# Optimization experiments

Hardware: AMD Instinct MI355X
Metric: run time of the kernel (lower is better)

## Reference

```python
import jax, jax.numpy as jnp
import numpy as np
from jax import lax

N, L, C_IN, NOISE_C, COMP, NC = 256, 512, 514, 112, 16, 2
MAIN_IN = NOISE_C + COMP  # 128
FEAT = NC * 4 * L         # 4096

def _conv1d(x, w, b, pad):
    # x [N,C,L], w [O,I,K]
    y = lax.conv_general_dilated(x, w, (1,), [(pad, pad)], dimension_numbers=('NCH', 'OIH', 'NCH'))
    return y + b[None, :, None]

def _bn(x, g, b):
    # BatchNorm1d, training mode: biased batch stats over (N, L)
    m = x.mean(axis=(0, 2), keepdims=True)
    v = x.var(axis=(0, 2), keepdims=True)
    return (x - m) * lax.rsqrt(v + 1e-5) * g[None, :, None] + b[None, :, None]

def _lrelu(x):
    return jnp.where(x >= 0, x, 0.2 * x)

def _pos_encode(length, dim):
    j = np.arange(dim)
    div = 1.0 / np.power(10000.0, 2 * (j[:, None] // 2) / dim)   # [dim,1]
    ang = np.arange(length)[None, :] * div                       # [dim,length]
    ang = np.where((j % 2 == 0)[:, None], np.sin(ang), np.cos(ang))
    return jnp.asarray(ang[None], jnp.float32)                   # [1,dim,length]

def _assemble(circle_prob, slider_prob):
    # Vectorized run-length label expansion equivalent to the per-sample python while-loop.
    # circle_prob [N, L/2, 2], slider_prob [N, L/4, 2] -> [N, L, 3]
    n, B = slider_prob.shape[0], slider_prob.shape[1]
    c = jnp.argmax(circle_prob, -1)
    s = jnp.argmax(slider_prob, -1)
    zc = jnp.zeros(circle_prob.shape[:-1] + (1,), circle_prob.dtype)
    zs = jnp.zeros(slider_prob.shape[:-1] + (1,), slider_prob.dtype)
    cp3 = jnp.concatenate([circle_prob, zc], -1)                                   # insert 0 at class 2
    sp3 = jnp.concatenate([slider_prob[..., :1], zs, slider_prob[..., 1:]], -1)    # insert 0 at class 1
    pad100 = jnp.array([1., 0., 0.], cp3.dtype)
    pad001 = jnp.array([0., 0., 1.], cp3.dtype)
    bidx = jnp.arange(B)[None, :]
    # slider-body blocks: slider run continues and not cut by sequence end
    body = (s == 1) & (bidx < B - 1)
    prev_body = jnp.concatenate([jnp.zeros((n, 1), bool), body[:, :-1]], 1)
    # tail block ends a slider run (either run stops, or boundary block)
    tail = ((s == 1) & (bidx == B - 1)) | ((s == 0) & prev_body)
    # circle emission for each half-step: prob row if predicted circle else pad
    cr0 = jnp.where((c == 1)[..., None], cp3, pad100).reshape(n, B, 2, 3)
    bodyE = body[..., None]
    row0 = jnp.where((body | tail)[..., None], sp3, cr0[:, :, 0, :])
    row1 = jnp.where(bodyE, pad001, pad100)
    row2 = jnp.where(bodyE, pad001, cr0[:, :, 1, :])
    row3 = jnp.where(bodyE, pad001, pad100)
    return jnp.stack([row0, row1, row2, row3], 2).reshape(n, 4 * B, 3)

def _forward(noise, cond_data, gumbel_u, ext_w1, ext_b1, ext_w2, ext_b2, ext_bn_g, ext_bn_b,
             m_w1, m_b1, m_w2, m_b2, m_bn_g, m_bn_b, lin_w, lin_b, circ_w, circ_b, slid_w, slid_b):
    # FeatureExtractor
    x = cond_data.transpose(0, 2, 1)                      # [N, 514, L]
    x = _lrelu(_conv1d(x, ext_w1, ext_b1, 0))             # [N, 32, L]
    cond = _bn(_conv1d(x, ext_w2, ext_b2, 1), ext_bn_g, ext_bn_b)  # [N, 16, L]
    gen_in = jnp.concatenate([cond, noise.transpose(0, 2, 1)], 1) + _pos_encode(L, MAIN_IN)  # [N,128,L]
    h = _lrelu(_conv1d(gen_in, m_w1, m_b1, 3))            # [N, 32, L]
    h = _lrelu(_bn(_conv1d(h, m_w2, m_b2, 1), m_bn_g, m_bn_b))     # [N, 8, L]
    flat = _lrelu(h.reshape(h.shape[0], -1) @ lin_w + lin_b)       # [N, 4096]
    circle_prob = (flat @ circ_w + circ_b).reshape(-1, L // 2, NC)
    slider_prob = (flat @ slid_w + slid_b).reshape(-1, L // 4, NC)
    out = _assemble(circle_prob, slider_prob)             # [N, L, 3]
    # gumbel_softmax(hard=True, tau=1)
    g = -jnp.log(-jnp.log(gumbel_u + 1e-10) + 1e-10)
    logits = out + g
    y_soft = jax.nn.softmax(logits, -1)
    y_hard = jax.nn.one_hot(jnp.argmax(logits, -1), 3, dtype=y_soft.dtype)
    gen_out = y_hard + y_soft - lax.stop_gradient(y_soft)
    return gen_out, cond

def setup_inputs() -> dict:
    key = jax.random.key(0)
    ks = jax.random.split(key, 12)
    def rn(k, shape, fan_in):
        return jax.random.normal(k, shape, jnp.float32) * (1.0 / fan_in) ** 0.5
    return {
        'noise': jax.random.normal(ks[0], (N, L, NOISE_C), jnp.float32),
        'cond_data': jax.random.normal(ks[1], (N, L, C_IN), jnp.float32),
        'gumbel_u': jax.random.uniform(ks[2], (N, L, 3), jnp.float32),
        'ext_w1': rn(ks[3], (C_IN // 16, C_IN, 1), C_IN), 'ext_b1': jnp.zeros(C_IN // 16),
        'ext_w2': rn(ks[4], (COMP, C_IN // 16, 3), 3 * (C_IN // 16)), 'ext_b2': jnp.zeros(COMP),
        'ext_bn_g': jnp.ones(COMP), 'ext_bn_b': jnp.zeros(COMP),
        'm_w1': rn(ks[5], (NC * 16, MAIN_IN, 7), 7 * MAIN_IN), 'm_b1': jnp.zeros(NC * 16),
        'm_w2': rn(ks[6], (NC * 4, NC * 16, 3), 3 * NC * 16), 'm_b2': jnp.zeros(NC * 4),
        'm_bn_g': jnp.ones(NC * 4), 'm_bn_b': jnp.zeros(NC * 4),
        'lin_w': rn(ks[7], (FEAT, FEAT), FEAT), 'lin_b': jnp.zeros(FEAT),
        'circ_w': rn(ks[8], (FEAT, NC * L // 2), FEAT), 'circ_b': jnp.zeros(NC * L // 2),
        'slid_w': rn(ks[9], (FEAT, NC * L // 4), FEAT), 'slid_b': jnp.zeros(NC * L // 4),
    }

def reference(noise, cond_data, gumbel_u, ext_w1, ext_b1, ext_w2, ext_b2, ext_bn_g, ext_bn_b,
              m_w1, m_b1, m_w2, m_b2, m_bn_g, m_bn_b, lin_w, lin_b, circ_w, circ_b, slid_w, slid_b):
    return _forward(noise, cond_data, gumbel_u, ext_w1, ext_b1, ext_w2, ext_b2, ext_bn_g, ext_bn_b,
                    m_w1, m_b1, m_w2, m_b2, m_bn_g, m_bn_b, lin_w, lin_b, circ_w, circ_b, slid_w, slid_b)
```

## Files before the change

kernel.cpp:

```cpp
#include <hip/hip_runtime.h>
#include <math.h>

#define NB 256
#define LL 512
#define CIN 514

__device__ __forceinline__ float lrelu(float x) { return x >= 0.f ? x : 0.2f * x; }

__global__ __launch_bounds__(256) void k_pos(float* __restrict__ pos) {
    int idx = blockIdx.x * 256 + threadIdx.x;
    int c = idx >> 9, l = idx & 511;
    double e = (double)(2 * (c >> 1)) / 128.0;
    double dv = 1.0 / pow(10000.0, e);
    double a = (double)l * dv;
    pos[idx] = (float)((c & 1) ? cos(a) : sin(a));
}

__global__ __launch_bounds__(256) void k_posconv(const float* __restrict__ POS, const float* __restrict__ W,
                                                 const float* __restrict__ bias, float* __restrict__ PC) {
    const int t = threadIdx.x;
    const int o = blockIdx.x >> 4, l0 = (blockIdx.x & 15) * 32;
    const int l = l0 + (t & 31), cs = t >> 5;
    float acc = 0.f;
    for (int ci = 0; ci < 16; ++ci) {
        int c = cs * 16 + ci;
        float wv[7];
#pragma unroll
        for (int k = 0; k < 7; ++k) wv[k] = W[o * 896 + c * 7 + k];
#pragma unroll
        for (int k = 0; k < 7; ++k) {
            int gl = l + k - 3;
            if (gl >= 0 && gl < LL) acc += wv[k] * POS[c * LL + gl];
        }
    }
    __shared__ float red[8][33];
    red[cs][t & 31] = acc;
    __syncthreads();
    if (cs == 0) {
        float s = bias[o];
#pragma unroll
        for (int j = 0; j < 8; ++j) s += red[j][t & 31];
        PC[o * LL + l0 + (t & 31)] = s;
    }
}

__global__ __launch_bounds__(256) void k_conv1(const float* __restrict__ X, const float* __restrict__ W,
                                               float* __restrict__ Pbase) {
    __shared__ __align__(16) float As[16][524];
    __shared__ __align__(16) float Bs[16][36];
    const int t = threadIdx.x;
    const int n = blockIdx.x >> 2, z = blockIdx.x & 3;
    const int kbase = z * 128;
    const int nch = (z == 3) ? 9 : 8;
    const int tl = t & 63, to = t >> 6;
    const size_t rowbase = (size_t)n * 512 * CIN;

    float acc[8][8];
#pragma unroll
    for (int oi = 0; oi < 8; ++oi)
#pragma unroll
        for (int p = 0; p < 8; ++p) acc[oi][p] = 0.f;

    float2 pf[16];
    float2 pfb;

    {
        const int kb = kbase;
#pragma unroll
        for (int ps = 0; ps < 16; ++ps) {
            int idx = ps * 256 + t;
            int pos = idx >> 3, kp = idx & 7;
            int gk = kb + kp * 2;
            float2 v = {0.f, 0.f};
            if (gk + 1 < CIN) v = *(const float2*)(X + rowbase + (size_t)pos * CIN + gk);
            else if (gk < CIN) v.x = X[rowbase + (size_t)pos * CIN + gk];
            pf[ps] = v;
        }
        {
            int o = t >> 3, kp = t & 7;
            int gk = kb + kp * 2;
            float2 v = {0.f, 0.f};
            if (gk + 1 < CIN) v = *(const float2*)(W + (size_t)o * CIN + gk);
            else if (gk < CIN) v.x = W[(size_t)o * CIN + gk];
            pfb = v;
        }
#pragma unroll
        for (int ps = 0; ps < 16; ++ps) {
            int idx = ps * 256 + t;
            int pos = idx >> 3, kp = idx & 7;
            As[kp * 2][pos] = pf[ps].x;
            As[kp * 2 + 1][pos] = pf[ps].y;
        }
        {
            int o = t >> 3, kp = t & 7;
            Bs[kp * 2][o] = pfb.x;
            Bs[kp * 2 + 1][o] = pfb.y;
        }
    }
    __syncthreads();

    for (int c = 0; c < nch; ++c) {
        if (c + 1 < nch) {
            const int kb = kbase + (c + 1) * 16;
#pragma unroll
            for (int ps = 0; ps < 16; ++ps) {
                int idx = ps * 256 + t;
                int pos = idx >> 3, kp = idx & 7;
                int gk = kb + kp * 2;
                float2 v = {0.f, 0.f};
                if (gk + 1 < CIN) v = *(const float2*)(X + rowbase + (size_t)pos * CIN + gk);
                else if (gk < CIN) v.x = X[rowbase + (size_t)pos * CIN + gk];
                pf[ps] = v;
            }
            int o = t >> 3, kp = t & 7;
            int gk = kb + kp * 2;
            float2 v = {0.f, 0.f};
            if (gk + 1 < CIN) v = *(const float2*)(W + (size_t)o * CIN + gk);
            else if (gk < CIN) v.x = W[(size_t)o * CIN + gk];
            pfb = v;
        }
#pragma unroll
        for (int kk = 0; kk < 16; ++kk) {
            float4 aL = *(const float4*)&As[kk][tl * 4];
            float4 aH = *(const float4*)&As[kk][256 + tl * 4];
            float4 b0 = *(const float4*)&Bs[kk][to * 8];
            float4 b1 = *(const float4*)&Bs[kk][to * 8 + 4];
            float av[8] = {aL.x, aL.y, aL.z, aL.w, aH.x, aH.y, aH.z, aH.w};
            float bv[8] = {b0.x, b0.y, b0.z, b0.w, b1.x, b1.y, b1.z, b1.w};
#pragma unroll
            for (int oi = 0; oi < 8; ++oi)
#pragma unroll
                for (int p = 0; p < 8; ++p) acc[oi][p] += av[p] * bv[oi];
        }
        __syncthreads();
        if (c + 1 < nch) {
#pragma unroll
            for (int ps = 0; ps < 16; ++ps) {
                int idx = ps * 256 + t;
                int pos = idx >> 3, kp = idx & 7;
                As[kp * 2][pos] = pf[ps].x;
                As[kp * 2 + 1][pos] = pf[ps].y;
            }
            int o = t >> 3, kp = t & 7;
            Bs[kp * 2][o] = pfb.x;
            Bs[kp * 2 + 1][o] = pfb.y;
        }
        __syncthreads();
    }

    float* P = Pbase + (size_t)z * 4194304;
#pragma unroll
    for (int oi = 0; oi < 8; ++oi) {
        int o = to * 8 + oi;
        float4 v0 = {acc[oi][0], acc[oi][1], acc[oi][2], acc[oi][3]};
        float4 v1 = {acc[oi][4], acc[oi][5], acc[oi][6], acc[oi][7]};
        *(float4*)(P + ((size_t)n * 32 + o) * LL + tl * 4) = v0;
        *(float4*)(P + ((size_t)n * 32 + o) * LL + 256 + tl * 4) = v1;
    }
}

__global__ __launch_bounds__(256) void k_conv2(const float* __restrict__ Pbase,
                                               const float* __restrict__ b1, const float* __restrict__ W,
                                               const float* __restrict__ bias, float* __restrict__ out) {
    __shared__ __align__(16) float Xs[32][264];
    __shared__ __align__(16) float Ws[16][32][4];
    const int t = threadIdx.x;
    const int n = blockIdx.x >> 1, l0 = (blockIdx.x & 1) * 256;
    for (int idx = t; idx < 32 * 258; idx += 256) {
        int i = idx / 258, j = idx % 258;
        int gl = l0 - 1 + j;
        float v = 0.f;
        if (gl >= 0 && gl < LL) {
            size_t off = ((size_t)n * 32 + i) * LL + gl;
            v = lrelu(Pbase[off] + Pbase[off + 4194304] + Pbase[off + 8388608] + Pbase[off + 12582912] + b1[i]);
        }
        Xs[i][j] = v;
    }
    for (int idx = t; idx < 1536; idx += 256) {
        int o = idx / 96, r = idx % 96;
        Ws[o][r / 3][r % 3] = W[idx];
    }
    __syncthreads();
    const int tx = t & 31, ty = t >> 5;
    float acc[2][8];
#pragma unroll
    for (int q = 0; q < 2; ++q)
#pragma unroll
        for (int p = 0; p < 8; ++p) acc[q][p] = 0.f;
    for (int i = 0; i < 32; ++i) {
        float4 a0 = *(const float4*)&Xs[i][tx*8];
        float4 a1 = *(const float4*)&Xs[i][tx*8+4];
        float4 a2 = *(const float4*)&Xs[i][tx*8+8];
        float a[12] = {a0.x,a0.y,a0.z,a0.w,a1.x,a1.y,a1.z,a1.w,a2.x,a2.y,a2.z,a2.w};
#pragma unroll
        for (int q = 0; q < 2; ++q) {
            float4 b = *(const float4*)&Ws[ty*2+q][i][0];
#pragma unroll
            for (int p = 0; p < 8; ++p)
                acc[q][p] += a[p]*b.x + a[p+1]*b.y + a[p+2]*b.z;
        }
    }
#pragma unroll
    for (int q = 0; q < 2; ++q) {
        int o = ty*2+q; float bb = bias[o];
#pragma unroll
        for (int h = 0; h < 2; ++h) {
            float4 v;
            v.x = acc[q][h*4+0] + bb; v.y = acc[q][h*4+1] + bb;
            v.z = acc[q][h*4+2] + bb; v.w = acc[q][h*4+3] + bb;
            *(float4*)(out + ((size_t)n*16 + o)*LL + l0 + tx*8 + h*4) = v;
        }
    }
}

__global__ __launch_bounds__(256) void k_redstats(const float* __restrict__ src, int C, float* __restrict__ part) {
    const int ch = blockIdx.x, sl = blockIdx.y, t = threadIdx.x;
    float s = 0.f, q = 0.f;
    for (int i = t; i < 4096; i += 256) {
        int n = sl*8 + (i >> 9), l = i & 511;
        float v = src[((size_t)n*C + ch)*LL + l];
        s += v; q += v*v;
    }
    __shared__ float rs[256], rq[256];
    rs[t] = s; rq[t] = q;
    __syncthreads();
    for (int off = 128; off > 0; off >>= 1) {
        if (t < off) { rs[t] += rs[t+off]; rq[t] += rq[t+off]; }
        __syncthreads();
    }
    if (t == 0) { part[(ch*32+sl)*2] = rs[0]; part[(ch*32+sl)*2+1] = rq[0]; }
}

__global__ void k_bnfinal(const float* __restrict__ part, const float* __restrict__ g,
                          const float* __restrict__ b, int C, float* __restrict__ ss) {
    int ch = threadIdx.x;
    if (ch >= C) return;
    float s = 0.f, q = 0.f;
    for (int j = 0; j < 32; ++j) { s += part[(ch*32 + j)*2]; q += part[(ch*32 + j)*2 + 1]; }
    float mean = s * (1.f/131072.f);
    float var = q * (1.f/131072.f) - mean*mean;
    float sc = g[ch] / sqrtf(var + 1e-5f);
    ss[ch] = sc;
    ss[C + ch] = b[ch] - mean * sc;
}

__global__ __launch_bounds__(256) void k_bnapply(const float* __restrict__ src, const float* __restrict__ ss,
        int C, float* __restrict__ dst, int act, int total4) {
    int i4 = blockIdx.x * 256 + threadIdx.x;
    if (i4 >= total4) return;
    int i = i4 << 2;
    int ch = (i >> 9) % C;
    float sc = ss[ch], sh = ss[C + ch];
    float4 v = reinterpret_cast<const float4*>(src)[i4];
    v.x = v.x*sc + sh; v.y = v.y*sc + sh; v.z = v.z*sc + sh; v.w = v.w*sc + sh;
    if (act) { v.x = lrelu(v.x); v.y = lrelu(v.y); v.z = lrelu(v.z); v.w = lrelu(v.w); }
    reinterpret_cast<float4*>(dst)[i4] = v;
}

__global__ __launch_bounds__(256) void k_mconv1(const float* __restrict__ C16, const float* __restrict__ NZ,
        const float* __restrict__ PC, const float* __restrict__ W,
        float* __restrict__ out0, float* __restrict__ out1) {
    __shared__ __align__(16) float Gs[16][268];
    __shared__ __align__(16) float Ws[32][16][8];
    const int t = threadIdx.x;
    const int n = blockIdx.x >> 2, l0 = ((blockIdx.x >> 1) & 1) * 256, z = blockIdx.x & 1;
    const int tx = t & 31, ty = t >> 5;
    float acc[4][8];
#pragma unroll
    for (int q = 0; q < 4; ++q)
#pragma unroll
        for (int p = 0; p < 8; ++p) acc[q][p] = 0.f;

    float gpf[17];
    float wpf[14];

    if (z == 0) {
        for (int idx = t; idx < 16*262; idx += 256) {
            int c = idx / 262, j = idx - c*262;
            int gl = l0 - 3 + j;
            float v = 0.f;
            if (gl >= 0 && gl < LL) v = C16[((size_t)n*16 + c)*LL + gl];
            Gs[c][j] = v;
        }
#pragma unroll
        for (int p = 0; p < 14; ++p) {
            int idx = p * 256 + t;
            int o = idx / 112, r = idx - o * 112;
            Ws[o][r / 7][r % 7] = W[(size_t)o*896 + r];
        }
    } else {
#pragma unroll
        for (int p = 0; p < 17; ++p) {
            int idx = p * 256 + t;
            float v = 0.f;
            if (idx < 4192) {
                int c = idx & 15, j = idx >> 4;
                int gl = l0 - 3 + j;
                if (gl >= 0 && gl < LL) v = NZ[((size_t)n*LL + gl)*112 + 48 + c];
            }
            gpf[p] = v;
        }
#pragma unroll
        for (int p = 0; p < 14; ++p) {
            int idx = p * 256 + t;
            int o = idx / 112, r = idx - o * 112;
            wpf[p] = W[(size_t)o*896 + 4*112 + r];
        }
#pragma unroll
        for (int p = 0; p < 17; ++p) {
            int idx = p * 256 + t;
            if (idx < 4192) Gs[idx & 15][idx >> 4] = gpf[p];
        }
#pragma unroll
        for (int p = 0; p < 14; ++p) {
            int idx = p * 256 + t;
            int o = idx / 112, r = idx - o * 112;
            Ws[o][r / 7][r % 7] = wpf[p];
        }
    }
    __syncthreads();

    for (int cc = 0; cc < 4; ++cc) {
        if (cc < 3) {
            const int nctg = z * 4 + cc + 1;
            const int nc0 = nctg * 16 - 16;
#pragma unroll
            for (int p = 0; p < 17; ++p) {
                int idx = p * 256 + t;
                float v = 0.f;
                if (idx < 4192) {
                    int c = idx & 15, j = idx >> 4;
                    int gl = l0 - 3 + j;
                    if (gl >= 0 && gl < LL) v = NZ[((size_t)n*LL + gl)*112 + nc0 + c];
                }
                gpf[p] = v;
            }
#pragma unroll
            for (int p = 0; p < 14; ++p) {
                int idx = p * 256 + t;
                int o = idx / 112, r = idx - o * 112;
                wpf[p] = W[(size_t)o*896 + nctg*112 + r];
            }
        }
        for (int ci = 0; ci < 16; ++ci) {
            float4 a0 = *(const float4*)&Gs[ci][tx*4];
            float4 a1 = *(const float4*)&Gs[ci][tx*4+4];
            float4 a2 = *(const float4*)&Gs[ci][tx*4+8];
            float4 a3 = *(const float4*)&Gs[ci][128+tx*4];
            float4 a4 = *(const float4*)&Gs[ci][128+tx*4+4];
            float4 a5 = *(const float4*)&Gs[ci][128+tx*4+8];
            float aA[12] = {a0.x,a0.y,a0.z,a0.w,a1.x,a1.y,a1.z,a1.w,a2.x,a2.y,a2.z,a2.w};
            float aB[12] = {a3.x,a3.y,a3.z,a3.w,a4.x,a4.y,a4.z,a4.w,a5.x,a5.y,a5.z,a5.w};
#pragma unroll
            for (int q = 0; q < 4; ++q) {
                float4 b0 = *(const float4*)&Ws[ty*4+q][ci][0];
                float4 b1 = *(const float4*)&Ws[ty*4+q][ci][4];
                float b[7] = {b0.x,b0.y,b0.z,b0.w,b1.x,b1.y,b1.z};
#pragma unroll
                for (int p = 0; p < 4; ++p) {
#pragma unroll
                    for (int k = 0; k < 7; ++k) {
                        acc[q][p]   += aA[p+k]*b[k];
                        acc[q][4+p] += aB[p+k]*b[k];
                    }
                }
            }
        }
        if (cc < 3) {
            __syncthreads();
#pragma unroll
            for (int p = 0; p < 17; ++p) {
                int idx = p * 256 + t;
                if (idx < 4192) Gs[idx & 15][idx >> 4] = gpf[p];
            }
#pragma unroll
            for (int p = 0; p < 14; ++p) {
                int idx = p * 256 + t;
                int o = idx / 112, r = idx - o * 112;
                Ws[o][r / 7][r % 7] = wpf[p];
            }
            __syncthreads();
        }
    }

    float* out = z ? out1 : out0;
#pragma unroll
    for (int q = 0; q < 4; ++q) {
        int o = ty*4 + q;
        float4 p0 = {0.f,0.f,0.f,0.f}, p1 = {0.f,0.f,0.f,0.f};
        if (z == 0) {
            p0 = *(const float4*)(PC + o*LL + l0 + tx*4);
            p1 = *(const float4*)(PC + o*LL + l0 + 128 + tx*4);
        }
        float4 v0 = {acc[q][0]+p0.x, acc[q][1]+p0.y, acc[q][2]+p0.z, acc[q][3]+p0.w};
        float4 v1 = {acc[q][4]+p1.x, acc[q][5]+p1.y, acc[q][6]+p1.z, acc[q][7]+p1.w};
        *(float4*)(out + ((size_t)n*32 + o)*LL + l0 + tx*4) = v0;
        *(float4*)(out + ((size_t)n*32 + o)*LL + l0 + 128 + tx*4) = v1;
    }
}

__global__ __launch_bounds__(256) void k_mconv2(const float* __restrict__ P0, const float* __restrict__ P1,
        const float* __restrict__ W, const float* __restrict__ bias, float* __restrict__ out) {
    __shared__ __align__(16) float Xs[32][264];
    __shared__ __align__(16) float Ws[8][32][4];
    const int t = threadIdx.x;
    const int n = blockIdx.x >> 1, l0 = (blockIdx.x & 1) * 256;
    for (int idx = t; idx < 32 * 258; idx += 256) {
        int i = idx / 258, j = idx % 258;
        int gl = l0 - 1 + j;
        float v = 0.f;
        if (gl >= 0 && gl < LL) {
            size_t off = ((size_t)n * 32 + i) * LL + gl;
            v = lrelu(P0[off] + P1[off]);
        }
        Xs[i][j] = v;
    }
    for (int idx = t; idx < 768; idx += 256) {
        int o = idx / 96, r = idx % 96;
        Ws[o][r / 3][r % 3] = W[idx];
    }
    __syncthreads();
    const int tx = t & 31, ty = t >> 5;
    float acc[8];
#pragma unroll
    for (int p = 0; p < 8; ++p) acc[p] = 0.f;
    for (int i = 0; i < 32; ++i) {
        float4 a0 = *(const float4*)&Xs[i][tx*8];
        float4 a1 = *(const float4*)&Xs[i][tx*8+4];
        float4 a2 = *(const float4*)&Xs[i][tx*8+8];
        float a[12] = {a0.x,a0.y,a0.z,a0.w,a1.x,a1.y,a1.z,a1.w,a2.x,a2.y,a2.z,a2.w};
        float4 b = *(const float4*)&Ws[ty][i][0];
#pragma unroll
        for (int p = 0; p < 8; ++p)
            acc[p] += a[p]*b.x + a[p+1]*b.y + a[p+2]*b.z;
    }
    float bb = bias[ty];
#pragma unroll
    for (int h = 0; h < 2; ++h) {
        float4 v;
        v.x = acc[h*4+0] + bb; v.y = acc[h*4+1] + bb;
        v.z = acc[h*4+2] + bb; v.w = acc[h*4+3] + bb;
        *(float4*)(out + ((size_t)n*8 + ty)*LL + l0 + tx*8 + h*4) = v;
    }
}

__global__ __launch_bounds__(256) void k_lin(const float* __restrict__ A, const float* __restrict__ B,
                                             float* __restrict__ part) {
    __shared__ __align__(16) float As[16][132];
    __shared__ __align__(16) float Bs[16][132];
    const int t = threadIdx.x;
    const int bid = blockIdx.x;
    const int xcd = bid & 7, j = bid >> 3;
    const int z = j >> 3;
    const int m0 = ((j >> 2) & 1) * 128;
    const int f0 = (xcd * 4 + (j & 3)) * 128;
    const int k0base = z * 256;
    const int sar = t & 127, saq = t >> 7;
    const int sbr = t >> 4, sbq = t & 15;
    const int mq = (t & 15) * 4, fq = (t >> 4) * 4;

    float acc[8][8];
#pragma unroll
    for (int i = 0; i < 8; ++i)
#pragma unroll
        for (int q = 0; q < 8; ++q) acc[i][q] = 0.f;

    for (int it = 0; it < 16; ++it) {
        const int k0 = k0base + it * 16;
        {
            const float* pA = A + (size_t)(m0 + sar) * 4096 + k0 + saq * 8;
            float4 a0 = *(const float4*)(pA);
            float4 a1 = *(const float4*)(pA + 4);
            const float* pB = B + (size_t)(k0 + sbr) * 4096 + f0 + sbq * 8;
            float4 b0 = *(const float4*)(pB);
            float4 b1 = *(const float4*)(pB + 4);
            As[saq*8+0][sar] = a0.x; As[saq*8+1][sar] = a0.y; As[saq*8+2][sar] = a0.z; As[saq*8+3][sar] = a0.w;
            As[saq*8+4][sar] = a1.x; As[saq*8+5][sar] = a1.y; As[saq*8+6][sar] = a1.z; As[saq*8+7][sar] = a1.w;
            *(float4*)&Bs[sbr][sbq*8] = b0;
            *(float4*)&Bs[sbr][sbq*8+4] = b1;
        }
        __syncthreads();
#pragma unroll
        for (int kk = 0; kk < 16; ++kk) {
            float4 a0 = *(const float4*)&As[kk][mq];
            float4 a1 = *(const float4*)&As[kk][mq + 64];
            float4 b0 = *(const float4*)&Bs[kk][fq];
            float4 b1 = *(const float4*)&Bs[kk][fq + 64];
            float av[8] = {a0.x,a0.y,a0.z,a0.w,a1.x,a1.y,a1.z,a1.w};
            float bv[8] = {b0.x,b0.y,b0.z,b0.w,b1.x,b1.y,b1.z,b1.w};
#pragma unroll
            for (int i = 0; i < 8; ++i)
#pragma unroll
                for (int q = 0; q < 8; ++q) acc[i][q] += av[i] * bv[q];
        }
        __syncthreads();
    }

#pragma unroll
    for (int i = 0; i < 8; ++i) {
        int m = m0 + mq + (i & 3) + (i >> 2) * 64;
        float4 v0 = {acc[i][0], acc[i][1], acc[i][2], acc[i][3]};
        float4 v1 = {acc[i][4], acc[i][5], acc[i][6], acc[i][7]};
        *(float4*)(part + ((size_t)z * 256 + m) * 4096 + f0 + fq) = v0;
        *(float4*)(part + ((size_t)z * 256 + m) * 4096 + f0 + fq + 64) = v1;
    }
}

__global__ __launch_bounds__(256) void k_linred(const float* __restrict__ part, const float* __restrict__ bias,
        float* __restrict__ out) {
    int i4 = blockIdx.x*256 + threadIdx.x;
    int i = i4 << 2;
    int f = i & 4095;
    float4 s = *(const float4*)(bias + f);
#pragma unroll
    for (int zz = 0; zz < 16; ++zz) {
        float4 p = ((const float4*)(part + (size_t)zz * 1048576))[i4];
        s.x += p.x; s.y += p.y; s.z += p.z; s.w += p.w;
    }
    float4 r;
    r.x = lrelu(s.x); r.y = lrelu(s.y); r.z = lrelu(s.z); r.w = lrelu(s.w);
    ((float4*)out)[i4] = r;
}

__global__ __launch_bounds__(256) void k_heads(const float* __restrict__ A, const float* __restrict__ CW,
        const float* __restrict__ SW, float* __restrict__ part) {
    __shared__ __align__(16) float As[32][36];
    __shared__ __align__(16) float Bs[32][132];
    const int t = threadIdx.x;
    const int m0 = blockIdx.x * 32, f0 = blockIdx.y * 128, z = blockIdx.z;
    const float* B; int ldb, fb;
    if (f0 < 512) { B = CW; ldb = 512; fb = f0; } else { B = SW; ldb = 256; fb = f0 - 512; }
    const int tm = t & 7, tf = t >> 3;
    const int mi = t >> 3, kq = t & 7;
    float acc[4][4];
#pragma unroll
    for (int pm = 0; pm < 4; ++pm)
#pragma unroll
        for (int pf = 0; pf < 4; ++pf) acc[pm][pf] = 0.f;
    for (int k0 = z * 256; k0 < z * 256 + 256; k0 += 32) {
        float4 av = *(const float4*)(A + (size_t)(m0 + mi) * 4096 + k0 + kq * 4);
        As[kq*4+0][mi] = av.x; As[kq*4+1][mi] = av.y; As[kq*4+2][mi] = av.z; As[kq*4+3][mi] = av.w;
#pragma unroll
        for (int pass = 0; pass < 4; ++pass) {
            int fi = pass * 32 + kq * 4;
            *(float4*)&Bs[mi][fi] = *(const float4*)(B + (size_t)(k0 + mi) * ldb + fb + fi);
        }
        __syncthreads();
#pragma unroll 8
        for (int kk = 0; kk < 32; ++kk) {
            float4 a = *(const float4*)&As[kk][tm * 4];
            float4 b = *(const float4*)&Bs[kk][tf * 4];
            float avv[4] = {a.x,a.y,a.z,a.w};
            float bvv[4] = {b.x,b.y,b.z,b.w};
#pragma unroll
            for (int pm = 0; pm < 4; ++pm)
#pragma unroll
                for (int pf = 0; pf < 4; ++pf) acc[pm][pf] += avv[pm]*bvv[pf];
        }
        __syncthreads();
    }
#pragma unroll
    for (int pm = 0; pm < 4; ++pm) {
        float4 v = {acc[pm][0], acc[pm][1], acc[pm][2], acc[pm][3]};
        *(float4*)(part + ((size_t)z * 256 + m0 + tm * 4 + pm) * 768 + f0 + tf * 4) = v;
    }
}

__global__ __launch_bounds__(256) void k_headred(const float* __restrict__ part, const float* __restrict__ cb,
        const float* __restrict__ sb, float* __restrict__ circ, float* __restrict__ slid) {
    int i4 = blockIdx.x * 256 + threadIdx.x;
    int i = i4 << 2;
    int n = i / 768, f = i % 768;
    float4 s = {0.f,0.f,0.f,0.f};
#pragma unroll
    for (int ks = 0; ks < 16; ++ks) {
        float4 p = *(const float4*)(part + ((size_t)ks*256 + n)*768 + f);
        s.x += p.x; s.y += p.y; s.z += p.z; s.w += p.w;
    }
    if (f < 512) {
        float4 bb = *(const float4*)(cb + f);
        s.x += bb.x; s.y += bb.y; s.z += bb.z; s.w += bb.w;
        *(float4*)(circ + (size_t)n*512 + f) = s;
    } else {
        float4 bb = *(const float4*)(sb + f - 512);
        s.x += bb.x; s.y += bb.y; s.z += bb.z; s.w += bb.w;
        *(float4*)(slid + (size_t)n*256 + f - 512) = s;
    }
}

__global__ __launch_bounds__(128) void k_assemble(const float* __restrict__ circ, const float* __restrict__ slid,
        const float* __restrict__ gum, float* __restrict__ out) {
    const int n = blockIdx.x;
    const int b = threadIdx.x;
    const float* sp = slid + (size_t)n * 256;
    const float* cp = circ + (size_t)n * 512;
    float sl0 = sp[2*b], sl1 = sp[2*b+1];
    int s = sl1 > sl0 ? 1 : 0;
    int prevb = 0;
    if (b > 0) prevb = (sp[2*b-1] > sp[2*b-2]) ? 1 : 0;
    bool body = (s == 1) && (b < 127);
    bool tail = ((s == 1) && (b == 127)) || ((s == 0) && (prevb == 1));
    float c0a = cp[4*b], c0b = cp[4*b+1], c1a = cp[4*b+2], c1b = cp[4*b+3];
    bool cA = c0b > c0a, cB = c1b > c1a;
    float rows[4][3];
    if (body || tail)      { rows[0][0]=sl0; rows[0][1]=0.f; rows[0][2]=sl1; }
    else if (cA)           { rows[0][0]=c0a; rows[0][1]=c0b; rows[0][2]=0.f; }
    else                   { rows[0][0]=1.f; rows[0][1]=0.f; rows[0][2]=0.f; }
    if (body)              { rows[1][0]=0.f; rows[1][1]=0.f; rows[1][2]=1.f; }
    else                   { rows[1][0]=1.f; rows[1][1]=0.f; rows[1][2]=0.f; }
    if (body)              { rows[2][0]=0.f; rows[2][1]=0.f; rows[2][2]=1.f; }
    else if (cB)           { rows[2][0]=c1a; rows[2][1]=c1b; rows[2][2]=0.f; }
    else                   { rows[2][0]=1.f; rows[2][1]=0.f; rows[2][2]=0.f; }
    rows[3][0]=rows[1][0]; rows[3][1]=rows[1][1]; rows[3][2]=rows[1][2];
#pragma unroll
    for (int r = 0; r < 4; ++r) {
        int l = 4*b + r;
        const float* u = gum + ((size_t)n*512 + l)*3;
        float g0 = -logf(-logf(u[0]+1e-10f)+1e-10f);
        float g1 = -logf(-logf(u[1]+1e-10f)+1e-10f);
        float g2 = -logf(-logf(u[2]+1e-10f)+1e-10f);
        float t0 = rows[r][0]+g0, t1 = rows[r][1]+g1, t2 = rows[r][2]+g2;
        int am = 0; float mv = t0;
        if (t1 > mv) { am = 1; mv = t1; }
        if (t2 > mv) { am = 2; mv = t2; }
        float e0 = expf(t0-mv), e1 = expf(t1-mv), e2 = expf(t2-mv);
        float ssum = e0+e1+e2;
        float y0 = e0/ssum, y1 = e1/ssum, y2 = e2/ssum;
        float* o = out + ((size_t)n*512 + l)*3;
        o[0] = ((am==0?1.f:0.f) + y0) - y0;
        o[1] = ((am==1?1.f:0.f) + y1) - y1;
        o[2] = ((am==2?1.f:0.f) + y2) - y2;
    }
}

extern "C" void kernel_launch(void* const* d_in, const int* in_sizes, int n_in,
                              void* d_out, int out_size, void* d_ws, size_t ws_size,
                              hipStream_t stream) {
    const float* noise   = (const float*)d_in[0];
    const float* cond    = (const float*)d_in[1];
    const float* gumbel  = (const float*)d_in[2];
    const float* ext_w1  = (const float*)d_in[3];
    const float* ext_b1  = (const float*)d_in[4];
    const float* ext_w2  = (const float*)d_in[5];
    const float* ext_b2  = (const float*)d_in[6];
    const float* ext_bng = (const float*)d_in[7];
    const float* ext_bnb = (const float*)d_in[8];
    const float* m_w1    = (const float*)d_in[9];
    const float* m_b1    = (const float*)d_in[10];
    const float* m_w2    = (const float*)d_in[11];
    const float* m_b2    = (const float*)d_in[12];
    const float* m_bng   = (const float*)d_in[13];
    const float* m_bnb   = (const float*)d_in[14];
    const float* lin_w   = (const float*)d_in[15];
    const float* lin_b   = (const float*)d_in[16];
    const float* circ_w  = (const float*)d_in[17];
    const float* circ_b  = (const float*)d_in[18];
    const float* slid_w  = (const float*)d_in[19];
    const float* slid_b  = (const float*)d_in[20];

    float* genout  = (float*)d_out;
    float* condout = (float*)d_out + 256*512*3;

    float* w     = (float*)d_ws;
    float* ws0   = w;
    float* y2    = ws0 + 16777216;
    float* posb  = y2 + 2097152;
    float* pc    = posb + 65536;
    float* circ  = pc + 16384;
    float* slid  = circ + 131072;
    float* flatB = slid + 65536;
    float* partH = flatB + 1048576;
    float* stats = partH + 3145728;

    k_pos<<<256, 256, 0, stream>>>(posb);
    k_posconv<<<512, 256, 0, stream>>>(posb, m_w1, m_b1, pc);
    k_conv1<<<1024, 256, 0, stream>>>(cond, ext_w1, ws0);
    k_conv2<<<512, 256, 0, stream>>>(ws0, ext_b1, ext_w2, ext_b2, y2);
    k_redstats<<<dim3(16,32), 256, 0, stream>>>(y2, 16, stats);
    k_bnfinal<<<1, 64, 0, stream>>>(stats, ext_bng, ext_bnb, 16, stats + 2048);
    k_bnapply<<<2048, 256, 0, stream>>>(y2, stats + 2048, 16, condout, 0, 524288);
    k_mconv1<<<1024, 256, 0, stream>>>(condout, noise, pc, m_w1, ws0, ws0 + 4194304);
    k_mconv2<<<512, 256, 0, stream>>>(ws0, ws0 + 4194304, m_w2, m_b2, y2);
    k_redstats<<<dim3(8,32), 256, 0, stream>>>(y2, 8, stats);
    k_bnfinal<<<1, 64, 0, stream>>>(stats, m_bng, m_bnb, 8, stats + 2048 + 64);
    k_bnapply<<<1024, 256, 0, stream>>>(y2, stats + 2048 + 64, 8, y2, 1, 262144);
    k_lin<<<1024, 256, 0, stream>>>(y2, lin_w, ws0);
    k_linred<<<1024, 256, 0, stream>>>(ws0, lin_b, flatB);
    k_heads<<<dim3(8,6,16), 256, 0, stream>>>(flatB, circ_w, slid_w, partH);
    k_headred<<<192, 256, 0, stream>>>(partH, circ_b, slid_b, circ, slid);
    k_assemble<<<256, 128, 0, stream>>>(circ, slid, gumbel, genout);
}
```

Baseline: 524.0 us.

## Double-buffer mconv1 channel chunks and fuse BN apply and head reduction

k_mconv1 now loads 8-channel chunks into double-buffered shared memory, which removes one barrier per chunk and the special first-chunk path but doubles the number of pipeline stages. The BatchNorm scale/shift and leaky ReLU for the main branch are applied while loading A inside k_lin, so the separate k_bnapply pass over y2 is no longer needed. The head partial-sum reduction is merged into k_assemble through shared memory, dropping the k_headred launch and its circ/slid intermediate buffers. The trade-offs are extra ALU work in the k_lin load path and a less parallel reduction in assemble, with only 256 blocks.

```diff
diff --git a/kernel.cpp b/kernel.cpp
--- a/kernel.cpp
+++ b/kernel.cpp
@@ -257,11 +257,46 @@
     reinterpret_cast<float4*>(dst)[i4] = v;
 }
 
+#define MC1_LOADG(hh) { \
+    int cb0 = z*64 + (hh)*8; \
+    _Pragma("unroll") \
+    for (int p = 0; p < 9; ++p) { \
+        int idx = p*256 + t; float v = 0.f; \
+        if (idx < 2096) { \
+            int c = idx & 7, jj = idx >> 3; int gl = l0 - 3 + jj; \
+            if (gl >= 0 && gl < LL) { \
+                if (z == 0 && (hh) < 2) v = C16[((size_t)n*16 + cb0 + c)*LL + gl]; \
+                else v = NZ[((size_t)n*LL + gl)*112 + cb0 - 16 + c]; \
+            } \
+        } \
+        gpf[p] = v; } }
+
+#define MC1_WRITEG(bb) { \
+    _Pragma("unroll") \
+    for (int p = 0; p < 9; ++p) { \
+        int idx = p*256 + t; \
+        if (idx < 2096) Gs[bb][idx & 7][idx >> 3] = gpf[p]; } }
+
+#define MC1_LOADW(hh) { \
+    int b7 = (z*64 + (hh)*8)*7; \
+    _Pragma("unroll") \
+    for (int p = 0; p < 8; ++p) { \
+        int idx = p*256 + t; \
+        int k = idx & 7, ci = (idx >> 3) & 7, o = idx >> 6; \
+        wpf[p] = (k < 7) ? W[(size_t)o*896 + b7 + ci*7 + k] : 0.f; } }
+
+#define MC1_WRITEW(bb) { \
+    _Pragma("unroll") \
+    for (int p = 0; p < 8; ++p) { \
+        int idx = p*256 + t; \
+        int k = idx & 7; \
+        if (k < 7) { int ci = (idx >> 3) & 7, o = idx >> 6; Ws[bb][o][ci][k] = wpf[p]; } } }
+
 __global__ __launch_bounds__(256) void k_mconv1(const float* __restrict__ C16, const float* __restrict__ NZ,
         const float* __restrict__ PC, const float* __restrict__ W,
         float* __restrict__ out0, float* __restrict__ out1) {
-    __shared__ __align__(16) float Gs[16][268];
-    __shared__ __align__(16) float Ws[32][16][8];
+    __shared__ __align__(16) float Gs[2][8][268];
+    __shared__ __align__(16) float Ws[2][32][8][8];
     const int t = threadIdx.x;
     const int n = blockIdx.x >> 2, l0 = ((blockIdx.x >> 1) & 1) * 256, z = blockIdx.x & 1;
     const int tx = t & 31, ty = t >> 5;
@@ -271,90 +306,34 @@
 #pragma unroll
         for (int p = 0; p < 8; ++p) acc[q][p] = 0.f;
 
-    float gpf[17];
-    float wpf[14];
-
-    if (z == 0) {
-        for (int idx = t; idx < 16*262; idx += 256) {
-            int c = idx / 262, j = idx - c*262;
-            int gl = l0 - 3 + j;
-            float v = 0.f;
-            if (gl >= 0 && gl < LL) v = C16[((size_t)n*16 + c)*LL + gl];
-            Gs[c][j] = v;
-        }
-#pragma unroll
-        for (int p = 0; p < 14; ++p) {
-            int idx = p * 256 + t;
-            int o = idx / 112, r = idx - o * 112;
-            Ws[o][r / 7][r % 7] = W[(size_t)o*896 + r];
-        }
-    } else {
-#pragma unroll
-        for (int p = 0; p < 17; ++p) {
-            int idx = p * 256 + t;
-            float v = 0.f;
-            if (idx < 4192) {
-                int c = idx & 15, j = idx >> 4;
-                int gl = l0 - 3 + j;
-                if (gl >= 0 && gl < LL) v = NZ[((size_t)n*LL + gl)*112 + 48 + c];
-            }
-            gpf[p] = v;
-        }
-#pragma unroll
-        for (int p = 0; p < 14; ++p) {
-            int idx = p * 256 + t;
-            int o = idx / 112, r = idx - o * 112;
-            wpf[p] = W[(size_t)o*896 + 4*112 + r];
-        }
-#pragma unroll
-        for (int p = 0; p < 17; ++p) {
-            int idx = p * 256 + t;
-            if (idx < 4192) Gs[idx & 15][idx >> 4] = gpf[p];
-        }
-#pragma unroll
-        for (int p = 0; p < 14; ++p) {
-            int idx = p * 256 + t;
-            int o = idx / 112, r = idx - o * 112;
-            Ws[o][r / 7][r % 7] = wpf[p];
-        }
-    }
+    float gpf[9];
+    float wpf[8];
+
+    MC1_LOADG(0)
+    MC1_LOADW(0)
+    MC1_WRITEG(0)
+    MC1_WRITEW(0)
     __syncthreads();
 
-    for (int cc = 0; cc < 4; ++cc) {
-        if (cc < 3) {
-            const int nctg = z * 4 + cc + 1;
-            const int nc0 = nctg * 16 - 16;
-#pragma unroll
-            for (int p = 0; p < 17; ++p) {
-                int idx = p * 256 + t;
-                float v = 0.f;
-                if (idx < 4192) {
-                    int c = idx & 15, j = idx >> 4;
-                    int gl = l0 - 3 + j;
-                    if (gl >= 0 && gl < LL) v = NZ[((size_t)n*LL + gl)*112 + nc0 + c];
-                }
-                gpf[p] = v;
-            }
-#pragma unroll
-            for (int p = 0; p < 14; ++p) {
-                int idx = p * 256 + t;
-                int o = idx / 112, r = idx - o * 112;
-                wpf[p] = W[(size_t)o*896 + nctg*112 + r];
-            }
-        }
-        for (int ci = 0; ci < 16; ++ci) {
-            float4 a0 = *(const float4*)&Gs[ci][tx*4];
-            float4 a1 = *(const float4*)&Gs[ci][tx*4+4];
-            float4 a2 = *(const float4*)&Gs[ci][tx*4+8];
-            float4 a3 = *(const float4*)&Gs[ci][128+tx*4];
-            float4 a4 = *(const float4*)&Gs[ci][128+tx*4+4];
-            float4 a5 = *(const float4*)&Gs[ci][128+tx*4+8];
+    for (int h = 0; h < 8; ++h) {
+        const int hb = h & 1;
+        if (h < 7) {
+            MC1_LOADG(h + 1)
+            MC1_LOADW(h + 1)
+        }
+        for (int ci = 0; ci < 8; ++ci) {
+            float4 a0 = *(const float4*)&Gs[hb][ci][tx*4];
+            float4 a1 = *(const float4*)&Gs[hb][ci][tx*4+4];
+            float4 a2 = *(const float4*)&Gs[hb][ci][tx*4+8];
+            float4 a3 = *(const float4*)&Gs[hb][ci][128+tx*4];
+            float4 a4 = *(const float4*)&Gs[hb][ci][128+tx*4+4];
+            float4 a5 = *(const float4*)&Gs[hb][ci][128+tx*4+8];
             float aA[12] = {a0.x,a0.y,a0.z,a0.w,a1.x,a1.y,a1.z,a1.w,a2.x,a2.y,a2.z,a2.w};
             float aB[12] = {a3.x,a3.y,a3.z,a3.w,a4.x,a4.y,a4.z,a4.w,a5.x,a5.y,a5.z,a5.w};
 #pragma unroll
             for (int q = 0; q < 4; ++q) {
-                float4 b0 = *(const float4*)&Ws[ty*4+q][ci][0];
-                float4 b1 = *(const float4*)&Ws[ty*4+q][ci][4];
+                float4 b0 = *(const float4*)&Ws[hb][ty*4+q][ci][0];
+                float4 b1 = *(const float4*)&Ws[hb][ty*4+q][ci][4];
                 float b[7] = {b0.x,b0.y,b0.z,b0.w,b1.x,b1.y,b1.z};
 #pragma unroll
                 for (int p = 0; p < 4; ++p) {
@@ -366,19 +345,10 @@
                 }
             }
         }
-        if (cc < 3) {
-            __syncthreads();
-#pragma unroll
-            for (int p = 0; p < 17; ++p) {
-                int idx = p * 256 + t;
-                if (idx < 4192) Gs[idx & 15][idx >> 4] = gpf[p];
-            }
-#pragma unroll
-            for (int p = 0; p < 14; ++p) {
-                int idx = p * 256 + t;
-                int o = idx / 112, r = idx - o * 112;
-                Ws[o][r / 7][r % 7] = wpf[p];
-            }
+        if (h < 7) {
+            const int nb = hb ^ 1;
+            MC1_WRITEG(nb)
+            MC1_WRITEW(nb)
             __syncthreads();
         }
     }
@@ -445,7 +415,7 @@
 }
 
 __global__ __launch_bounds__(256) void k_lin(const float* __restrict__ A, const float* __restrict__ B,
-                                             float* __restrict__ part) {
+                                             const float* __restrict__ SS, float* __restrict__ part) {
     __shared__ __align__(16) float As[16][132];
     __shared__ __align__(16) float Bs[16][132];
     const int t = threadIdx.x;
@@ -468,9 +438,16 @@
     for (int it = 0; it < 16; ++it) {
         const int k0 = k0base + it * 16;
         {
-            const float* pA = A + (size_t)(m0 + sar) * 4096 + k0 + saq * 8;
+            const int ka = k0 + saq * 8;
+            const int ch = ka >> 9;
+            const float sc = SS[ch], sh = SS[8 + ch];
+            const float* pA = A + (size_t)(m0 + sar) * 4096 + ka;
             float4 a0 = *(const float4*)(pA);
             float4 a1 = *(const float4*)(pA + 4);
+            a0.x = lrelu(a0.x*sc + sh); a0.y = lrelu(a0.y*sc + sh);
+            a0.z = lrelu(a0.z*sc + sh); a0.w = lrelu(a0.w*sc + sh);
+            a1.x = lrelu(a1.x*sc + sh); a1.y = lrelu(a1.y*sc + sh);
+            a1.z = lrelu(a1.z*sc + sh); a1.w = lrelu(a1.w*sc + sh);
             const float* pB = B + (size_t)(k0 + sbr) * 4096 + f0 + sbq * 8;
             float4 b0 = *(const float4*)(pB);
             float4 b1 = *(const float4*)(pB + 4);
@@ -566,34 +543,25 @@
     }
 }
 
-__global__ __launch_bounds__(256) void k_headred(const float* __restrict__ part, const float* __restrict__ cb,
-        const float* __restrict__ sb, float* __restrict__ circ, float* __restrict__ slid) {
-    int i4 = blockIdx.x * 256 + threadIdx.x;
-    int i = i4 << 2;
-    int n = i / 768, f = i % 768;
-    float4 s = {0.f,0.f,0.f,0.f};
-#pragma unroll
-    for (int ks = 0; ks < 16; ++ks) {
-        float4 p = *(const float4*)(part + ((size_t)ks*256 + n)*768 + f);
-        s.x += p.x; s.y += p.y; s.z += p.z; s.w += p.w;
-    }
-    if (f < 512) {
-        float4 bb = *(const float4*)(cb + f);
-        s.x += bb.x; s.y += bb.y; s.z += bb.z; s.w += bb.w;
-        *(float4*)(circ + (size_t)n*512 + f) = s;
-    } else {
-        float4 bb = *(const float4*)(sb + f - 512);
-        s.x += bb.x; s.y += bb.y; s.z += bb.z; s.w += bb.w;
-        *(float4*)(slid + (size_t)n*256 + f - 512) = s;
-    }
-}
-
-__global__ __launch_bounds__(128) void k_assemble(const float* __restrict__ circ, const float* __restrict__ slid,
-        const float* __restrict__ gum, float* __restrict__ out) {
+__global__ __launch_bounds__(256) void k_assemble(const float* __restrict__ part, const float* __restrict__ cb,
+        const float* __restrict__ sb, const float* __restrict__ gum, float* __restrict__ out) {
+    __shared__ float buf[768];
     const int n = blockIdx.x;
-    const int b = threadIdx.x;
-    const float* sp = slid + (size_t)n * 256;
-    const float* cp = circ + (size_t)n * 512;
+    const int t = threadIdx.x;
+#pragma unroll
+    for (int rep = 0; rep < 3; ++rep) {
+        int f = rep * 256 + t;
+        float s = 0.f;
+#pragma unroll
+        for (int ks = 0; ks < 16; ++ks) s += part[((size_t)(ks * 256 + n)) * 768 + f];
+        s += (f < 512) ? cb[f] : sb[f - 512];
+        buf[f] = s;
+    }
+    __syncthreads();
+    if (t >= 128) return;
+    const int b = t;
+    const float* cp = buf;
+    const float* sp = buf + 512;
     float sl0 = sp[2*b], sl1 = sp[2*b+1];
     int s = sl1 > sl0 ? 1 : 0;
     int prevb = 0;
@@ -666,9 +634,7 @@
     float* y2    = ws0 + 16777216;
     float* posb  = y2 + 2097152;
     float* pc    = posb + 65536;
-    float* circ  = pc + 16384;
-    float* slid  = circ + 131072;
-    float* flatB = slid + 65536;
+    float* flatB = pc + 16384;
     float* partH = flatB + 1048576;
     float* stats = partH + 3145728;
 
@@ -683,10 +649,8 @@
     k_mconv2<<<512, 256, 0, stream>>>(ws0, ws0 + 4194304, m_w2, m_b2, y2);
     k_redstats<<<dim3(8,32), 256, 0, stream>>>(y2, 8, stats);
     k_bnfinal<<<1, 64, 0, stream>>>(stats, m_bng, m_bnb, 8, stats + 2048 + 64);
-    k_bnapply<<<1024, 256, 0, stream>>>(y2, stats + 2048 + 64, 8, y2, 1, 262144);
-    k_lin<<<1024, 256, 0, stream>>>(y2, lin_w, ws0);
+    k_lin<<<1024, 256, 0, stream>>>(y2, lin_w, stats + 2048 + 64, ws0);
     k_linred<<<1024, 256, 0, stream>>>(ws0, lin_b, flatB);
     k_heads<<<dim3(8,6,16), 256, 0, stream>>>(flatB, circ_w, slid_w, partH);
-    k_headred<<<192, 256, 0, stream>>>(partH, circ_b, slid_b, circ, slid);
-    k_assemble<<<256, 128, 0, stream>>>(circ, slid, gumbel, genout);
-}
+    k_assemble<<<256, 256, 0, stream>>>(partH, circ_b, slid_b, gumbel, genout);
+}
```

After: 536.3 us. +2.3%, slower.
